# Kernel optimization log

Hardware: AMD Instinct MI355X
Metric: run time of the kernel (lower is better)

## Reference

```python
import jax, jax.numpy as jnp
import numpy as np

N, T, D, H = 4, 2048, 1024, 16
DH = D // H
NEG = -1e20


def setup_inputs() -> dict:
    key = jax.random.key(0)
    ks = jax.random.split(key, 6)
    std = 1.0 / np.sqrt(D)
    return {
        "query": jax.random.normal(ks[0], (N, T, D), jnp.float32),
        "mask": jax.random.randint(ks[1], (N, T), 0, 2, jnp.int32),
        "Wq": jax.random.normal(ks[2], (D, D), jnp.float32) * std,
        "bq": jnp.zeros((D,), jnp.float32),
        "Wk": jax.random.normal(ks[3], (D, D), jnp.float32) * std,
        "bk": jnp.zeros((D,), jnp.float32),
        "Wv": jax.random.normal(ks[4], (D, D), jnp.float32) * std,
        "bv": jnp.zeros((D,), jnp.float32),
        "Wo": jax.random.normal(ks[5], (D, D), jnp.float32) * std,
        "bo": jnp.zeros((D,), jnp.float32),
    }


def _heads(x):
    # [N,T,D] -> [N,H,T,DH]
    n, t, _ = x.shape
    return x.reshape(n, t, H, DH).transpose(0, 2, 1, 3)


def reference(query, mask, Wq, bq, Wk, bk, Wv, bv, Wo, bo):
    scale = jnp.asarray(np.sqrt(DH), query.dtype)
    q = _heads(query @ Wq.T + bq)
    k = _heads(query @ Wk.T + bk)  # self-attention: key = value = query
    v = _heads(query @ Wv.T + bv)
    dot = jnp.einsum("nhtd,nhsd->nhts", q, k)  # [N,H,T,T_k]
    # 2D mask [N,T] aligns by name to the QUERY axis: (N,1,T,1)
    attn_mask = (mask == 0)[:, None, :, None]
    dot = jnp.where(attn_mask, jnp.asarray(NEG, dot.dtype), dot)
    # faithful to source: scale applied AFTER masked_fill, inside softmax arg
    attn = jax.nn.softmax(dot / scale, axis=-1)
    ctx = jnp.einsum("nhts,nhsd->nhtd", attn, v)  # [N,H,T,DH]
    ctx = ctx.transpose(0, 2, 1, 3).reshape(query.shape[0], query.shape[1], D)
    return ctx @ Wo.T + bo
```

## Files before the change

### kernel.cpp

```cpp
#include <hip/hip_runtime.h>

typedef _Float16 f16;
typedef __attribute__((ext_vector_type(8))) _Float16 half8;
typedef __attribute__((ext_vector_type(4))) _Float16 half4;
typedef __attribute__((ext_vector_type(4))) float f32x4;
typedef __attribute__((ext_vector_type(16))) float f32x16;

#define DEVINL __device__ __forceinline__

constexpr int NBATCH = 4, T = 2048, D = 1024, H = 16, DH = 64;
constexpr int M = NBATCH * T;
constexpr float SCL2 = 0.18033688011f;

DEVINL void async16(const f16* g, f16* l) {
  __builtin_amdgcn_global_load_lds(
      (__attribute__((address_space(1))) void*)(g),
      (__attribute__((address_space(3))) void*)(l), 16, 0, 0);
}

DEVINL unsigned pk2(float x, float y) {
  auto h = __builtin_amdgcn_cvt_pkrtz(x, y);
  return __builtin_bit_cast(unsigned, h);
}

union H8U {
  half8 h;
  unsigned u[4];
};

__global__ void cvt_all_kernel(const float* __restrict__ query,
                               const float* __restrict__ wq, const float* __restrict__ wk,
                               const float* __restrict__ wv, const float* __restrict__ wo,
                               f16* __restrict__ dst) {
  constexpr int NQ4 = M * D / 4;
  constexpr int NW4 = D * D / 4;
  constexpr int NT4 = NQ4 + 4 * NW4;
  const float* srcs[4] = {wq, wk, wv, wo};
  int i = blockIdx.x * blockDim.x + threadIdx.x;
  int stride = gridDim.x * blockDim.x;
  for (; i < NT4; i += stride) {
    const float* s;
    int off;
    if (i < NQ4) { s = query; off = i; }
    else {
      int j = i - NQ4;
      s = srcs[j >> 18];
      off = j & (NW4 - 1);
    }
    float4 v = reinterpret_cast<const float4*>(s)[off];
    half4 h = {(f16)v.x, (f16)v.y, (f16)v.z, (f16)v.w};
    reinterpret_cast<half4*>(dst)[i] = h;
  }
}

template<bool F32OUT>
DEVINL void gemm_body(const f16* __restrict__ A, const f16* __restrict__ W,
                      const float* __restrict__ bias, void* __restrict__ out,
                      f16* As, f16* Bs, long bm, long bn, float oscale) {
  constexpr int K = 1024, BK = 64, NCOL = 1024;
  const int tid = threadIdx.x;
  const int lane = tid & 63, wave = tid >> 6;
  const int wr = wave >> 1, wc = wave & 1;
  const int srow = tid >> 3;
  const int sc = tid & 7;
  const int scol = ((sc ^ (srow & 7)) * 8);
  const f16* gA = A + (bm + srow) * (long)K + scol;
  const f16* gB = W + (bn + srow) * (long)K + scol;
  const int ldst = tid * 8;
  const int fr = lane & 15, hi4 = lane >> 4;
  f32x4 acc[4][4] = {};

  for (int k0 = 0; k0 < K; k0 += BK) {
#pragma unroll
    for (int c = 0; c < 4; ++c) {
      async16(gA + k0 + (long)(c * 32) * K, As + c * 2048 + ldst);
      async16(gB + k0 + (long)(c * 32) * K, Bs + c * 2048 + ldst);
    }
    __syncthreads();
#pragma unroll
    for (int kk = 0; kk < 2; ++kk) {
      half8 af[4], bf[4];
#pragma unroll
      for (int m = 0; m < 4; ++m) {
        const int ar = wr * 64 + m * 16 + fr;
        af[m] = *(const half8*)&As[ar * 64 + (((kk * 4 + hi4) ^ (ar & 7)) * 8)];
      }
#pragma unroll
      for (int n = 0; n < 4; ++n) {
        const int br = wc * 64 + n * 16 + fr;
        bf[n] = *(const half8*)&Bs[br * 64 + (((kk * 4 + hi4) ^ (br & 7)) * 8)];
      }
#pragma unroll
      for (int m = 0; m < 4; ++m)
#pragma unroll
        for (int n = 0; n < 4; ++n)
          acc[m][n] = __builtin_amdgcn_mfma_f32_16x16x32_f16(af[m], bf[n], acc[m][n], 0, 0, 0);
    }
    __syncthreads();
  }
  const int rq = hi4 * 4;
#pragma unroll
  for (int m = 0; m < 4; ++m) {
    const long row = bm + wr * 64 + m * 16 + rq;
#pragma unroll
    for (int n = 0; n < 4; ++n) {
      const long col = bn + wc * 64 + n * 16 + fr;
      const float bb = bias[col];
#pragma unroll
      for (int r = 0; r < 4; ++r) {
        float v = (acc[m][n][r] + bb) * oscale;
        if (F32OUT) ((float*)out)[(row + r) * (long)NCOL + col] = v;
        else        ((f16*)out)[(row + r) * (long)NCOL + col] = (f16)v;
      }
    }
  }
}

__global__ __launch_bounds__(256) void gemm_qkv(const f16* __restrict__ A,
                                                const f16* __restrict__ Wall,
                                                const float* __restrict__ bq,
                                                const float* __restrict__ bk,
                                                const float* __restrict__ bv,
                                                f16* __restrict__ Qh,
                                                f16* __restrict__ Kh,
                                                f16* __restrict__ Vh) {
  __shared__ __align__(16) f16 As[128 * 64];
  __shared__ __align__(16) f16 Bs[128 * 64];
  const int lin = (int)((blockIdx.z * gridDim.y + blockIdx.y) * gridDim.x + blockIdx.x);
  const int xcd = lin & 7;
  const int r = lin >> 3;
  const int by = xcd * 8 + (r & 7);
  const int bx = (r >> 3) & 7;
  const int z = r >> 6;
  const f16* W = Wall + (size_t)z * D * D;
  const float* bias = z == 0 ? bq : (z == 1 ? bk : bv);
  f16* out = z == 0 ? Qh : (z == 1 ? Kh : Vh);
  const float oscale = z == 0 ? SCL2 : 1.0f;
  gemm_body<false>(A, W, bias, (void*)out, As, Bs,
                   (long)by * 128, (long)bx * 128, oscale);
}

__global__ __launch_bounds__(256) void gemm_out(const f16* __restrict__ A,
                                                const f16* __restrict__ W,
                                                const float* __restrict__ bias,
                                                float* __restrict__ out) {
  __shared__ __align__(16) f16 As[128 * 64];
  __shared__ __align__(16) f16 Bs[128 * 64];
  const int lin = (int)(blockIdx.y * gridDim.x + blockIdx.x);
  const int xcd = lin & 7;
  const int r = lin >> 3;
  const int by = xcd * 8 + (r & 7);
  const int bx = r >> 3;
  gemm_body<true>(A, W, bias, (void*)out, As, Bs,
                  (long)by * 128, (long)bx * 128, 1.0f);
}

__global__ __launch_bounds__(512, 4) void attn_kernel(const f16* __restrict__ Qh,
                                                      const f16* __restrict__ Kh,
                                                      const f16* __restrict__ Vh,
                                                      const int* __restrict__ mask,
                                                      f16* __restrict__ Ch) {
  constexpr int NT = T / 64;
  constexpr int LDV = 72;
  constexpr int NWG = (T / 256) * NBATCH * H;
  __shared__ __align__(16) f16 smem[18432];
  f16* Ksb0 = smem;
  f16* Ksb1 = smem + 4096;
  f16* Vtb0 = smem + 8192;
  f16* Vtb1 = smem + 8192 + 4608;

  const int lin = (int)(blockIdx.y * gridDim.x + blockIdx.x);
  const int nid = (lin & 7) * (NWG / 8) + (lin >> 3);
  const int nh = nid >> 3;
  const int qt0 = (nid & 7) * 256;

  const int bn = nh >> 4;
  const int bh = nh & 15;
  const int tid = threadIdx.x, lane = tid & 63, wave = tid >> 6;
  const int q = lane & 31, hi = lane >> 5;

  const long base = ((long)bn * T) * D + (long)bh * DH;
  const int qrow = qt0 + wave * 32 + q;

  const bool pm = mask[bn * T + qrow] != 0;
  half8 qf[4];
#pragma unroll
  for (int f = 0; f < 4; ++f) {
    qf[f] = *(const half8*)&Qh[base + (long)qrow * D + f * 16 + hi * 8];
    if (!pm) qf[f] = half8{};
  }

  f32x16 o0 = {}, o1 = {}, lacc = {};
  const f16 onev = (f16)1.0f;
  const half8 ones8 = {onev, onev, onev, onev, onev, onev, onev, onev};

  const int skey = tid >> 3;
  const int sc = tid & 7;
  const int kcol = ((sc ^ (skey & 7)) * 8);
  const f16* ksrc = Kh + base + (long)skey * D + kcol;

  const int vs = lane;
  const int vd = wave * 8;
  const f16* vsrc = Vh + base + (long)vs * D + vd;

  async16(ksrc, Ksb0 + tid * 8);
  half8 va = *(const half8*)(vsrc);
  {
#pragma unroll
    for (int j = 0; j < 8; ++j) Vtb0[(vd + j) * LDV + vs] = va[j];
  }
  __syncthreads();

  for (int it = 0; it < NT; ++it) {
    const int cur = it & 1;
    f16* KsC = cur ? Ksb1 : Ksb0;
    f16* VtC = cur ? Vtb1 : Vtb0;
    f16* KsN = cur ? Ksb0 : Ksb1;
    f16* VtN = cur ? Vtb0 : Vtb1;

    if (it + 1 < NT) {
      const long koff = (long)(it + 1) * 64 * D;
      async16(ksrc + koff, KsN + tid * 8);
      va = *(const half8*)(vsrc + koff);
    }

    f32x16 s0 = {}, s1 = {};
    __builtin_amdgcn_s_setprio(1);
#pragma unroll
    for (int f = 0; f < 4; ++f) {
      const int ck = f * 2 + hi;
      half8 k0 = *(const half8*)&KsC[q * 64 + ((ck ^ (q & 7)) * 8)];
      half8 k1 = *(const half8*)&KsC[(32 + q) * 64 + ((ck ^ (q & 7)) * 8)];
      s0 = __builtin_amdgcn_mfma_f32_32x32x16_f16(k0, qf[f], s0, 0, 0, 0);
      s1 = __builtin_amdgcn_mfma_f32_32x32x16_f16(k1, qf[f], s1, 0, 0, 0);
    }
    __builtin_amdgcn_s_setprio(0);

#pragma unroll
    for (int r = 0; r < 16; ++r) {
      s0[r] = __builtin_amdgcn_exp2f(s0[r]);
      s1[r] = __builtin_amdgcn_exp2f(s1[r]);
    }

    half8 pf[4];
#pragma unroll
    for (int g = 0; g < 4; ++g) {
      float p0, p1, p2, p3, p4, p5, p6, p7;
      if (g == 0) { p0=s0[0];p1=s0[1];p2=s0[2];p3=s0[3];p4=s0[4];p5=s0[5];p6=s0[6];p7=s0[7]; }
      else if (g == 1) { p0=s0[8];p1=s0[9];p2=s0[10];p3=s0[11];p4=s0[12];p5=s0[13];p6=s0[14];p7=s0[15]; }
      else if (g == 2) { p0=s1[0];p1=s1[1];p2=s1[2];p3=s1[3];p4=s1[4];p5=s1[5];p6=s1[6];p7=s1[7]; }
      else { p0=s1[8];p1=s1[9];p2=s1[10];p3=s1[11];p4=s1[12];p5=s1[13];p6=s1[14];p7=s1[15]; }
      unsigned A0 = pk2(p0, p1), A1 = pk2(p2, p3);
      unsigned B0 = pk2(p4, p5), B1 = pk2(p6, p7);
      asm("v_permlane32_swap_b32 %0, %1" : "+v"(A0), "+v"(B0));
      asm("v_permlane32_swap_b32 %0, %1" : "+v"(A1), "+v"(B1));
      H8U u;
      u.u[0] = A0;
      u.u[1] = A1;
      u.u[2] = B0;
      u.u[3] = B1;
      pf[g] = u.h;
    }

    half8 psum = (pf[0] + pf[1]) + (pf[2] + pf[3]);

    __builtin_amdgcn_s_setprio(1);
#pragma unroll
    for (int kc = 0; kc < 4; ++kc) {
      half8 v0f = *(const half8*)&VtC[q * LDV + kc * 16 + hi * 8];
      half8 v1f = *(const half8*)&VtC[(32 + q) * LDV + kc * 16 + hi * 8];
      o0 = __builtin_amdgcn_mfma_f32_32x32x16_f16(v0f, pf[kc], o0, 0, 0, 0);
      o1 = __builtin_amdgcn_mfma_f32_32x32x16_f16(v1f, pf[kc], o1, 0, 0, 0);
    }
    lacc = __builtin_amdgcn_mfma_f32_32x32x16_f16(ones8, psum, lacc, 0, 0, 0);
    __builtin_amdgcn_s_setprio(0);

    if (it + 1 < NT) {
#pragma unroll
      for (int j = 0; j < 8; ++j) VtN[(vd + j) * LDV + vs] = va[j];
    }
    __syncthreads();
  }

  constexpr int EPL = 72;
  const float rl = 1.0f / lacc[0];
  f16* ep = smem + wave * 2304;
#pragma unroll
  for (int r = 0; r < 16; r += 2) {
    const int dd = (r & 3) + 8 * (r >> 2) + 4 * hi;
    *(unsigned*)&ep[q * EPL + dd]      = pk2(o0[r] * rl, o0[r + 1] * rl);
    *(unsigned*)&ep[q * EPL + 32 + dd] = pk2(o1[r] * rl, o1[r + 1] * rl);
  }
  asm volatile("s_waitcnt lgkmcnt(0)" ::: "memory");
  const int rr = lane >> 1, cw = lane & 1;
  const long orow = base + (long)(qt0 + wave * 32 + rr) * D + cw * 32;
#pragma unroll
  for (int c2 = 0; c2 < 4; ++c2) {
    half8 val = *(const half8*)&ep[rr * EPL + cw * 32 + c2 * 8];
    *(half8*)&Ch[orow + c2 * 8] = val;
  }
}

extern "C" void kernel_launch(void* const* d_in, const int* in_sizes, int n_in,
                              void* d_out, int out_size, void* d_ws, size_t ws_size,
                              hipStream_t stream) {
  const float* query = (const float*)d_in[0];
  const int*   mask  = (const int*)d_in[1];
  const float* Wq = (const float*)d_in[2];
  const float* bq = (const float*)d_in[3];
  const float* Wk = (const float*)d_in[4];
  const float* bk = (const float*)d_in[5];
  const float* Wv = (const float*)d_in[6];
  const float* bv = (const float*)d_in[7];
  const float* Wo = (const float*)d_in[8];
  const float* bo = (const float*)d_in[9];

  char* ws = (char*)d_ws;
  const size_t MD = (size_t)M * D;
  f16* Xh = (f16*)ws;
  f16* Wh = (f16*)(ws + (16u << 20));
  f16* Qh = (f16*)(ws + (24u << 20));
  f16 *KhP, *VhP;
  const size_t need = (24u << 20) + 3 * MD * sizeof(f16);
  if (ws_size >= need) {
    KhP = Qh + MD; VhP = KhP + MD;
  } else {
    KhP = (f16*)d_out; VhP = KhP + MD;
  }
  f16* Ch = Xh;

  cvt_all_kernel<<<dim3(2048), dim3(256), 0, stream>>>(query, Wq, Wk, Wv, Wo, Xh);

  gemm_qkv<<<dim3(8, 64, 3), dim3(256), 0, stream>>>(Xh, Wh, bq, bk, bv, Qh, KhP, VhP);

  attn_kernel<<<dim3(T / 256, NBATCH * H), dim3(512), 0, stream>>>(Qh, KhP, VhP, mask, Ch);

  gemm_out<<<dim3(8, 64), dim3(256), 0, stream>>>(Ch, Wh + 3 * (size_t)D * D, bo, (float*)d_out);
}
```

Baseline: 168.5 us.

## Double-buffer GEMM LDS tiles with async prefetch two stages ahead

The QKV and output projection GEMMs now use two LDS buffers. Global-to-LDS async loads for step t+2 are issued after the fragments for step t have been read into registers, with vmcnt waits instead of a full sync each iteration. This is meant to hide global load latency behind the MFMA work. In exchange it doubles LDS per block to 64KB, which may reduce occupancy, and it relies on hand-placed waitcnt and barrier ordering.

```diff
diff --git a/kernel.cpp b/kernel.cpp
--- a/kernel.cpp
+++ b/kernel.cpp
@@ -57,7 +57,8 @@
 DEVINL void gemm_body(const f16* __restrict__ A, const f16* __restrict__ W,
                       const float* __restrict__ bias, void* __restrict__ out,
                       f16* As, f16* Bs, long bm, long bn, float oscale) {
-  constexpr int K = 1024, BK = 64, NCOL = 1024;
+  constexpr int K = 1024, BK = 64, NCOL = 1024, BUF = 128 * 64;
+  constexpr int NSTEP = K / BK;
   const int tid = threadIdx.x;
   const int lane = tid & 63, wave = tid >> 6;
   const int wr = wave >> 1, wc = wave & 1;
@@ -70,34 +71,54 @@
   const int fr = lane & 15, hi4 = lane >> 4;
   f32x4 acc[4][4] = {};
 
-  for (int k0 = 0; k0 < K; k0 += BK) {
-#pragma unroll
-    for (int c = 0; c < 4; ++c) {
-      async16(gA + k0 + (long)(c * 32) * K, As + c * 2048 + ldst);
-      async16(gB + k0 + (long)(c * 32) * K, Bs + c * 2048 + ldst);
-    }
-    __syncthreads();
+#define GSTAGE(K0, AD, BD)                                                      \
+  {                                                                             \
+    _Pragma("unroll")                                                           \
+    for (int c = 0; c < 4; ++c) {                                               \
+      async16(gA + (K0) + (long)(c * 32) * K, (AD) + c * 2048 + ldst);          \
+      async16(gB + (K0) + (long)(c * 32) * K, (BD) + c * 2048 + ldst);          \
+    }                                                                           \
+  }
+
+  GSTAGE(0, As, Bs)
+  GSTAGE(BK, As + BUF, Bs + BUF)
+
+  for (int t = 0; t < NSTEP; ++t) {
+    if (t < NSTEP - 1) asm volatile("s_waitcnt vmcnt(8)" ::: "memory");
+    else               asm volatile("s_waitcnt vmcnt(0)" ::: "memory");
+    __builtin_amdgcn_s_barrier();
+    const f16* as_ = As + (t & 1) * BUF;
+    const f16* bs_ = Bs + (t & 1) * BUF;
+    half8 af[2][4], bf[2][4];
 #pragma unroll
     for (int kk = 0; kk < 2; ++kk) {
-      half8 af[4], bf[4];
 #pragma unroll
       for (int m = 0; m < 4; ++m) {
         const int ar = wr * 64 + m * 16 + fr;
-        af[m] = *(const half8*)&As[ar * 64 + (((kk * 4 + hi4) ^ (ar & 7)) * 8)];
+        af[kk][m] = *(const half8*)&as_[ar * 64 + (((kk * 4 + hi4) ^ (ar & 7)) * 8)];
       }
 #pragma unroll
       for (int n = 0; n < 4; ++n) {
         const int br = wc * 64 + n * 16 + fr;
-        bf[n] = *(const half8*)&Bs[br * 64 + (((kk * 4 + hi4) ^ (br & 7)) * 8)];
+        bf[kk][n] = *(const half8*)&bs_[br * 64 + (((kk * 4 + hi4) ^ (br & 7)) * 8)];
       }
+    }
+    asm volatile("s_waitcnt lgkmcnt(0)" ::: "memory");
+    __builtin_amdgcn_sched_barrier(0);
+    __builtin_amdgcn_s_barrier();
+    if (t + 2 < NSTEP) {
+      GSTAGE((t + 2) * BK, As + (t & 1) * BUF, Bs + (t & 1) * BUF)
+    }
+#pragma unroll
+    for (int kk = 0; kk < 2; ++kk)
 #pragma unroll
       for (int m = 0; m < 4; ++m)
 #pragma unroll
         for (int n = 0; n < 4; ++n)
-          acc[m][n] = __builtin_amdgcn_mfma_f32_16x16x32_f16(af[m], bf[n], acc[m][n], 0, 0, 0);
-    }
-    __syncthreads();
-  }
+          acc[m][n] = __builtin_amdgcn_mfma_f32_16x16x32_f16(af[kk][m], bf[kk][n], acc[m][n], 0, 0, 0);
+  }
+#undef GSTAGE
+
   const int rq = hi4 * 4;
 #pragma unroll
   for (int m = 0; m < 4; ++m) {
@@ -124,8 +145,8 @@
                                                 f16* __restrict__ Qh,
                                                 f16* __restrict__ Kh,
                                                 f16* __restrict__ Vh) {
-  __shared__ __align__(16) f16 As[128 * 64];
-  __shared__ __align__(16) f16 Bs[128 * 64];
+  __shared__ __align__(16) f16 As[2 * 128 * 64];
+  __shared__ __align__(16) f16 Bs[2 * 128 * 64];
   const int lin = (int)((blockIdx.z * gridDim.y + blockIdx.y) * gridDim.x + blockIdx.x);
   const int xcd = lin & 7;
   const int r = lin >> 3;
@@ -144,8 +165,8 @@
                                                 const f16* __restrict__ W,
                                                 const float* __restrict__ bias,
                                                 float* __restrict__ out) {
-  __shared__ __align__(16) f16 As[128 * 64];
-  __shared__ __align__(16) f16 Bs[128 * 64];
+  __shared__ __align__(16) f16 As[2 * 128 * 64];
+  __shared__ __align__(16) f16 Bs[2 * 128 * 64];
   const int lin = (int)(blockIdx.y * gridDim.x + blockIdx.x);
   const int xcd = lin & 7;
   const int r = lin >> 3;
```

After: 161.2 us (median of 2 runs). -4.3%, faster.
